# Kernel optimization log

Measured on AMD Instinct MI355X. Metric: run time of the kernel, lower is better.

The kernel has to match this reference:

```python
import jax, jax.numpy as jnp
import numpy as np
import math

HID = 4096
SLOTS = 8
HEADS = 8
BD = 512  # bottleneck_dim
HD = BD // HEADS  # effective head dim = 64
B, S = 4, 4096


def setup_inputs() -> dict:
    key = jax.random.key(0)
    ks = jax.random.split(key, 8)
    std = 1.0 / math.sqrt(HID)
    return {
        "hidden_states": jax.random.normal(ks[0], (B, S, HID), dtype=jnp.float32),
        "attention_mask": jax.random.randint(ks[1], (B, S), 0, 2, dtype=jnp.int32),
        "memory_slots": jax.random.normal(ks[2], (SLOTS, HID), dtype=jnp.float32) * std,
        # torch nn.Linear weights are [out_features, in_features]
        "Wq": jax.random.normal(ks[3], (BD, HID), dtype=jnp.float32) * std,
        "Wk": jax.random.normal(ks[4], (BD, HID), dtype=jnp.float32) * std,
        "Wv": jax.random.normal(ks[5], (BD, HID), dtype=jnp.float32) * std,
        "Wo": jax.random.normal(ks[6], (HID, BD), dtype=jnp.float32) * (1.0 / math.sqrt(BD)),
    }


def reference(hidden_states, attention_mask, memory_slots, Wq, Wk, Wv, Wo):
    # Q from learnable slots (same for every batch element): [slots, BD]
    Q = memory_slots @ Wq.T
    Q = Q.reshape(SLOTS, HEADS, HD)                      # n h d
    # K/V from sequence: [b, s, BD] -> [b, s, h, d]
    K = jnp.einsum('bsi,oi->bso', hidden_states, Wk).reshape(B, S, HEADS, HD)
    V = jnp.einsum('bsi,oi->bso', hidden_states, Wv).reshape(B, S, HEADS, HD)
    # scores: [b, h, n, s]
    scores = jnp.einsum('nhd,bshd->bhns', Q, K) / jnp.sqrt(jnp.array(HD, scores_dtype := jnp.float32))
    mask = attention_mask[:, None, None, :]              # [b,1,1,s]
    scores = jnp.where(mask == 0, jnp.finfo(scores.dtype).min, scores)
    attn = jax.nn.softmax(scores, axis=-1)
    # output: [b, n, h, d] -> [b, n, BD]
    out = jnp.einsum('bhns,bshd->bnhd', attn, V).reshape(B, SLOTS, BD)
    # o_proj back to hidden_size
    return jnp.einsum('bnd,od->bno', out, Wo)            # [b, slots, HID]
```

## Files before the change

### kernel.cpp

```cpp
#include <hip/hip_runtime.h>
#include <math.h>

#define HID   4096
#define SLOTS 8
#define HEADS 8
#define BD    512
#define HD    64
#define BB    4
#define SS    4096
#define R64   64
#define LSTR  72
#define KC    1024
#define NKZ   4
#define NT    16

typedef __attribute__((ext_vector_type(8))) short bf16x8;
typedef __attribute__((ext_vector_type(4))) float f32x4;

__device__ __forceinline__ unsigned short f2bf(float x) {
  unsigned int u = __builtin_bit_cast(unsigned int, x);
  return (unsigned short)((u + 0x7fffu + ((u >> 16) & 1u)) >> 16);
}

__device__ __forceinline__ void gl16(const void* g, void* l) {
  __builtin_amdgcn_global_load_lds(
      (const __attribute__((address_space(1))) unsigned int*)g,
      (__attribute__((address_space(3))) unsigned int*)l, 16, 0, 0);
}

__global__ __launch_bounds__(256) void hsb_kernel(const float* __restrict__ hs,
                                                  unsigned short* __restrict__ hsb) {
  const size_t total = (size_t)BB * SS * HID / 8;
  size_t stride = (size_t)gridDim.x * blockDim.x;
  for (size_t u = (size_t)blockIdx.x * blockDim.x + threadIdx.x; u < total; u += stride) {
    const float* src = hs + u * 8;
    float4 a = *(const float4*)src;
    float4 b = *(const float4*)(src + 4);
    union { unsigned short us[8]; uint4 q; } o;
    o.us[0] = f2bf(a.x); o.us[1] = f2bf(a.y); o.us[2] = f2bf(a.z); o.us[3] = f2bf(a.w);
    o.us[4] = f2bf(b.x); o.us[5] = f2bf(b.y); o.us[6] = f2bf(b.z); o.us[7] = f2bf(b.w);
    *(uint4*)(hsb + u * 8) = o.q;
  }
}

__global__ void q_kernel(const float* __restrict__ ms, const float* __restrict__ Wq,
                         float* __restrict__ Q) {
  int w = (blockIdx.x * blockDim.x + threadIdx.x) >> 6;
  int lane = threadIdx.x & 63;
  if (w >= SLOTS * BD) return;
  int n = w >> 9, o = w & (BD - 1);
  const float* a = ms + n * HID;
  const float* b = Wq + (size_t)o * HID;
  float acc = 0.f;
  for (int i = lane; i < HID; i += 64) acc = fmaf(a[i], b[i], acc);
  #pragma unroll
  for (int off = 32; off; off >>= 1) acc += __shfl_down(acc, off, 64);
  if (lane == 0) Q[w] = acc;
}

__global__ void qw_kernel(const float* __restrict__ Q, const float* __restrict__ Wk,
                          unsigned short* __restrict__ QW) {
  int idx = blockIdx.x * blockDim.x + threadIdx.x;
  int r = idx >> 12, i = idx & (HID - 1);
  int h = r >> 3, n = r & 7;
  const float* q  = Q + n * BD + h * HD;
  const float* wk = Wk + (size_t)(h * HD) * HID + i;
  float acc = 0.f;
  #pragma unroll 8
  for (int d = 0; d < HD; ++d) acc = fmaf(q[d], wk[(size_t)d * HID], acc);
  QW[idx] = f2bf(acc * 0.125f);
}

__global__ __launch_bounds__(256) void scores_mfma(const unsigned short* __restrict__ hsb,
                                                   const unsigned short* __restrict__ QW,
                                                   float* __restrict__ sp) {
  __shared__ __align__(16) unsigned short As[2][4096];
  __shared__ __align__(16) unsigned short Bs[2][4096];
  const int stile = blockIdx.x, b = blockIdx.y, kz = blockIdx.z;
  const int tid = threadIdx.x;
  const int wv = tid >> 6, lane = tid & 63;
  const int quad = lane >> 4, l16 = lane & 15;
  const int trow = tid >> 3;
  const int tslot = (tid & 7) << 4;
  const int scol = tslot ^ ((trow & 7) << 4);
  const char* aSrc0 = (const char*)hsb +
      (((size_t)(b * SS + stile * 64 + trow)) * HID + kz * KC) * 2 + scol;
  const char* aSrc1 = (const char*)hsb +
      (((size_t)(b * SS + stile * 64 + 32 + trow)) * HID + kz * KC) * 2 + scol;
  const char* bSrc0 = (const char*)QW + (((size_t)trow) * HID + kz * KC) * 2 + scol;
  const char* bSrc1 = (const char*)QW + (((size_t)(32 + trow)) * HID + kz * KC) * 2 + scol;

  f32x4 acc[4] = {};
  gl16(aSrc0, &As[0][tid * 8]);
  gl16(aSrc1, &As[0][2048 + tid * 8]);
  gl16(bSrc0, &Bs[0][tid * 8]);
  gl16(bSrc1, &Bs[0][2048 + tid * 8]);
  __syncthreads();

  const int sw = (l16 & 7) << 4;
  for (int c = 0; c < NT; ++c) {
    const int cur = c & 1, nxt = cur ^ 1;
    if (c < NT - 1) {
      const size_t off = (size_t)(c + 1) * 128;
      gl16(aSrc0 + off, &As[nxt][tid * 8]);
      gl16(aSrc1 + off, &As[nxt][2048 + tid * 8]);
      gl16(bSrc0 + off, &Bs[nxt][tid * 8]);
      gl16(bSrc1 + off, &Bs[nxt][2048 + tid * 8]);
    }
    const char* ab = (const char*)&As[cur][0];
    const char* bb = (const char*)&Bs[cur][0];
    #pragma unroll
    for (int ks = 0; ks < 2; ++ks) {
      bf16x8 bfrag = *(const bf16x8*)(bb + (wv * 16 + l16) * 128 + ((ks * 64 + quad * 16) ^ sw));
      #pragma unroll
      for (int mt = 0; mt < 4; ++mt) {
        bf16x8 afrag = *(const bf16x8*)(ab + (mt * 16 + l16) * 128 + ((ks * 64 + quad * 16) ^ sw));
        acc[mt] = __builtin_amdgcn_mfma_f32_16x16x32_bf16(afrag, bfrag, acc[mt], 0, 0, 0);
      }
    }
    __syncthreads();
  }
  const int r = wv * 16 + l16;
  #pragma unroll
  for (int mt = 0; mt < 4; ++mt) {
    int s = stile * 64 + mt * 16 + quad * 4;
    float4 v = make_float4(acc[mt][0], acc[mt][1], acc[mt][2], acc[mt][3]);
    *(float4*)(sp + ((size_t)((kz * BB + b) * R64 + r)) * SS + s) = v;
  }
}

__global__ __launch_bounds__(256) void softmax_kernel(const float* __restrict__ sp,
                                                      const int* __restrict__ mask,
                                                      unsigned short* __restrict__ attn) {
  int br = blockIdx.x;
  int b = br >> 6;
  int tid = threadIdx.x;
  const float* p0 = sp + ((size_t)(0 * BB * R64) + br) * SS;
  const float* p1 = sp + ((size_t)(1 * BB * R64) + br) * SS;
  const float* p2 = sp + ((size_t)(2 * BB * R64) + br) * SS;
  const float* p3 = sp + ((size_t)(3 * BB * R64) + br) * SS;
  const int* mrow = mask + b * SS;
  float vals[16];
  float mx = -INFINITY;
  #pragma unroll
  for (int j = 0; j < 16; ++j) {
    int s = tid + j * 256;
    float v = p0[s] + p1[s] + p2[s] + p3[s];
    if (mrow[s] == 0) v = -INFINITY;
    vals[j] = v;
    mx = fmaxf(mx, v);
  }
  __shared__ float redm[4], reds[4];
  #pragma unroll
  for (int off = 32; off; off >>= 1) mx = fmaxf(mx, __shfl_down(mx, off, 64));
  if ((tid & 63) == 0) redm[tid >> 6] = mx;
  __syncthreads();
  mx = fmaxf(fmaxf(redm[0], redm[1]), fmaxf(redm[2], redm[3]));
  float sum = 0.f;
  #pragma unroll
  for (int j = 0; j < 16; ++j) { vals[j] = expf(vals[j] - mx); sum += vals[j]; }
  #pragma unroll
  for (int off = 32; off; off >>= 1) sum += __shfl_down(sum, off, 64);
  if ((tid & 63) == 0) reds[tid >> 6] = sum;
  __syncthreads();
  sum = reds[0] + reds[1] + reds[2] + reds[3];
  float inv = 1.f / sum;
  #pragma unroll
  for (int j = 0; j < 16; ++j)
    attn[(size_t)br * SS + tid + j * 256] = f2bf(vals[j] * inv);
}

__global__ __launch_bounds__(256) void ctx_mfma(const unsigned short* __restrict__ attn,
                                                const unsigned short* __restrict__ hsb,
                                                float* __restrict__ ctxp) {
  __shared__ __align__(16) unsigned short As[2][4096];
  __shared__ __align__(16) unsigned short Bs[2][64 * LSTR];
  const int itile = blockIdx.x, b = blockIdx.y, kz = blockIdx.z;
  const int tid = threadIdx.x;
  const int wv = tid >> 6, lane = tid & 63;
  const int quad = lane >> 4, l16 = lane & 15;
  const int trow = tid >> 3;
  const int tslot = (tid & 7) << 4;
  const int scol = tslot ^ ((trow & 7) << 4);
  const char* aSrc0 = (const char*)attn +
      (((size_t)(b * R64 + trow)) * SS + kz * KC) * 2 + scol;
  const char* aSrc1 = (const char*)attn +
      (((size_t)(b * R64 + 32 + trow)) * SS + kz * KC) * 2 + scol;
  const int p = tid & 31, g = tid >> 5;
  const unsigned short* hb = hsb + ((size_t)(b * SS + kz * KC + 2 * p)) * HID + itile * 64 + g * 8;

  f32x4 acc[4] = {};
  uint4 h0 = *(const uint4*)(hb);
  uint4 h1 = *(const uint4*)(hb + HID);
  gl16(aSrc0, &As[0][tid * 8]);
  gl16(aSrc1, &As[0][2048 + tid * 8]);
  {
    const unsigned short* u0 = (const unsigned short*)&h0;
    const unsigned short* u1 = (const unsigned short*)&h1;
    unsigned int* bs32 = (unsigned int*)&Bs[0][0];
    #pragma unroll
    for (int j = 0; j < 8; ++j)
      bs32[(g * 8 + j) * (LSTR / 2) + p] = (unsigned int)u0[j] | ((unsigned int)u1[j] << 16);
  }
  h0 = *(const uint4*)(hb + (size_t)64 * HID);
  h1 = *(const uint4*)(hb + (size_t)65 * HID);
  __syncthreads();

  const int sw = (l16 & 7) << 4;
  for (int c = 0; c < NT; ++c) {
    const int cur = c & 1, nxt = cur ^ 1;
    if (c < NT - 1) {
      const size_t off = (size_t)(c + 1) * 128;
      gl16(aSrc0 + off, &As[nxt][tid * 8]);
      gl16(aSrc1 + off, &As[nxt][2048 + tid * 8]);
      const unsigned short* u0 = (const unsigned short*)&h0;
      const unsigned short* u1 = (const unsigned short*)&h1;
      unsigned int* bs32 = (unsigned int*)&Bs[nxt][0];
      #pragma unroll
      for (int j = 0; j < 8; ++j)
        bs32[(g * 8 + j) * (LSTR / 2) + p] = (unsigned int)u0[j] | ((unsigned int)u1[j] << 16);
      if (c < NT - 2) {
        const unsigned short* hn = hb + (size_t)(c + 2) * 64 * HID;
        h0 = *(const uint4*)(hn);
        h1 = *(const uint4*)(hn + HID);
      }
    }
    const char* ab = (const char*)&As[cur][0];
    #pragma unroll
    for (int ks = 0; ks < 2; ++ks) {
      bf16x8 bfrag = *(const bf16x8*)&Bs[cur][(wv * 16 + l16) * LSTR + ks * 32 + quad * 8];
      #pragma unroll
      for (int mt = 0; mt < 4; ++mt) {
        bf16x8 afrag = *(const bf16x8*)(ab + (mt * 16 + l16) * 128 + ((ks * 64 + quad * 16) ^ sw));
        acc[mt] = __builtin_amdgcn_mfma_f32_16x16x32_bf16(afrag, bfrag, acc[mt], 0, 0, 0);
      }
    }
    __syncthreads();
  }
  const int i = itile * 64 + wv * 16 + l16;
  #pragma unroll
  for (int mt = 0; mt < 4; ++mt) {
    int r0 = mt * 16 + quad * 4;
    #pragma unroll
    for (int j = 0; j < 4; ++j)
      ctxp[((size_t)((kz * BB + b) * R64 + r0 + j)) * HID + i] = acc[mt][j];
  }
}

__global__ void ctxsum_kernel(const float* __restrict__ ctxp, float* __restrict__ ctxs) {
  int idx = blockIdx.x * blockDim.x + threadIdx.x;
  const size_t n4 = (size_t)BB * R64 * HID / 4;
  if ((size_t)idx >= n4) return;
  const float4* a = (const float4*)ctxp;
  float4 v0 = a[idx];
  float4 v1 = a[idx + n4];
  float4 v2 = a[idx + 2 * n4];
  float4 v3 = a[idx + 3 * n4];
  float4 r = make_float4(v0.x + v1.x + v2.x + v3.x, v0.y + v1.y + v2.y + v3.y,
                         v0.z + v1.z + v2.z + v3.z, v0.w + v1.w + v2.w + v3.w);
  ((float4*)ctxs)[idx] = r;
}

__global__ void out_kernel(const float* __restrict__ ctx, const float* __restrict__ Wv,
                           float* __restrict__ out) {
  int w = (blockIdx.x * blockDim.x + threadIdx.x) >> 6;
  int lane = threadIdx.x & 63;
  if (w >= BB * BD) return;
  int b = w >> 9, hd = w & 511, h = hd >> 6;
  const float* wvp = Wv + (size_t)hd * HID;
  const float* cb  = ctx + ((size_t)b * R64 + h * 8) * HID;
  float acc[8] = {};
  for (int i = lane; i < HID; i += 64) {
    float wv = wvp[i];
    #pragma unroll
    for (int n = 0; n < 8; ++n) acc[n] = fmaf(cb[(size_t)n * HID + i], wv, acc[n]);
  }
  #pragma unroll
  for (int n = 0; n < 8; ++n) {
    float a = acc[n];
    #pragma unroll
    for (int off = 32; off; off >>= 1) a += __shfl_down(a, off, 64);
    if (lane == 0) out[((size_t)(b * SLOTS + n)) * BD + hd] = a;
  }
}

__global__ void final_kernel(const float* __restrict__ out, const float* __restrict__ Wo,
                             float* __restrict__ y) {
  int w = (blockIdx.x * blockDim.x + threadIdx.x) >> 6;
  int lane = threadIdx.x & 63;
  if (w >= HID) return;
  const float* wo = Wo + (size_t)w * BD;
  float wreg[8];
  #pragma unroll
  for (int j = 0; j < 8; ++j) wreg[j] = wo[lane + j * 64];
  for (int bn = 0; bn < BB * SLOTS; ++bn) {
    const float* orow = out + bn * BD;
    float acc = 0.f;
    #pragma unroll
    for (int j = 0; j < 8; ++j) acc = fmaf(orow[lane + j * 64], wreg[j], acc);
    #pragma unroll
    for (int off = 32; off; off >>= 1) acc += __shfl_down(acc, off, 64);
    if (lane == 0) y[(size_t)bn * HID + w] = acc;
  }
}

extern "C" void kernel_launch(void* const* d_in, const int* in_sizes, int n_in,
                              void* d_out, int out_size, void* d_ws, size_t ws_size,
                              hipStream_t stream) {
  const float* hs   = (const float*)d_in[0];
  const int*   mask = (const int*)d_in[1];
  const float* ms   = (const float*)d_in[2];
  const float* Wq   = (const float*)d_in[3];
  const float* Wk   = (const float*)d_in[4];
  const float* Wv   = (const float*)d_in[5];
  const float* Wo   = (const float*)d_in[6];

  char* ws = (char*)d_ws;
  float*          Q    = (float*)ws;          ws += 4096 * 4;
  unsigned short* QW   = (unsigned short*)ws; ws += R64 * HID * 2;
  unsigned short* hsb  = (unsigned short*)ws; ws += (size_t)BB * SS * HID * 2;
  float*          sp   = (float*)ws;          ws += (size_t)NKZ * BB * R64 * SS * 4;
  unsigned short* attn = (unsigned short*)ws; ws += (size_t)BB * R64 * SS * 2;
  float*          ctxp = (float*)ws;          ws += (size_t)NKZ * BB * R64 * HID * 4;
  float*          ctxs = (float*)ws;          ws += (size_t)BB * R64 * HID * 4;
  float*          out  = (float*)ws;

  hsb_kernel<<<dim3(2048), 256, 0, stream>>>(hs, hsb);
  q_kernel<<<dim3((SLOTS * BD * 64) / 256), 256, 0, stream>>>(ms, Wq, Q);
  qw_kernel<<<dim3((R64 * HID) / 256), 256, 0, stream>>>(Q, Wk, QW);
  scores_mfma<<<dim3(64, 4, 4), 256, 0, stream>>>(hsb, QW, sp);
  softmax_kernel<<<dim3(BB * R64), 256, 0, stream>>>(sp, mask, attn);
  ctx_mfma<<<dim3(64, 4, 4), 256, 0, stream>>>(attn, hsb, ctxp);
  ctxsum_kernel<<<dim3((BB * R64 * HID / 4) / 256), 256, 0, stream>>>(ctxp, ctxs);
  out_kernel<<<dim3((BB * BD * 64) / 256), 256, 0, stream>>>(ctxs, Wv, out);
  final_kernel<<<dim3((HID * 64) / 256), 256, 0, stream>>>(out, Wo, (float*)d_out);
}
```

Baseline: 551.5 us.

## Fuse bf16 conversion into scores GEMM and fold ctx partial sum into out

Removes the standalone fp32-to-bf16 conversion pass. The scores GEMM now loads fp32 hidden states through registers, converts them, writes them into swizzled LDS, and also writes the bf16 copy out for the later ctx GEMM. Removes the ctxsum kernel by having out_kernel add the four split-K partials inline. This saves one full read-write pass over the large activation tensor and two launches. In exchange the A operand no longer uses async global-to-LDS loads, so load latency is exposed through registers, and out_kernel reads four times more ctx data.

```diff
diff --git a/kernel.cpp b/kernel.cpp
--- a/kernel.cpp
+++ b/kernel.cpp
@@ -28,21 +28,6 @@
       (__attribute__((address_space(3))) unsigned int*)l, 16, 0, 0);
 }
 
-__global__ __launch_bounds__(256) void hsb_kernel(const float* __restrict__ hs,
-                                                  unsigned short* __restrict__ hsb) {
-  const size_t total = (size_t)BB * SS * HID / 8;
-  size_t stride = (size_t)gridDim.x * blockDim.x;
-  for (size_t u = (size_t)blockIdx.x * blockDim.x + threadIdx.x; u < total; u += stride) {
-    const float* src = hs + u * 8;
-    float4 a = *(const float4*)src;
-    float4 b = *(const float4*)(src + 4);
-    union { unsigned short us[8]; uint4 q; } o;
-    o.us[0] = f2bf(a.x); o.us[1] = f2bf(a.y); o.us[2] = f2bf(a.z); o.us[3] = f2bf(a.w);
-    o.us[4] = f2bf(b.x); o.us[5] = f2bf(b.y); o.us[6] = f2bf(b.z); o.us[7] = f2bf(b.w);
-    *(uint4*)(hsb + u * 8) = o.q;
-  }
-}
-
 __global__ void q_kernel(const float* __restrict__ ms, const float* __restrict__ Wq,
                          float* __restrict__ Q) {
   int w = (blockIdx.x * blockDim.x + threadIdx.x) >> 6;
@@ -71,8 +56,9 @@
   QW[idx] = f2bf(acc * 0.125f);
 }
 
-__global__ __launch_bounds__(256) void scores_mfma(const unsigned short* __restrict__ hsb,
+__global__ __launch_bounds__(256) void scores_mfma(const float* __restrict__ hs,
                                                    const unsigned short* __restrict__ QW,
+                                                   unsigned short* __restrict__ hsb,
                                                    float* __restrict__ sp) {
   __shared__ __align__(16) unsigned short As[2][4096];
   __shared__ __align__(16) unsigned short Bs[2][4096];
@@ -80,32 +66,66 @@
   const int tid = threadIdx.x;
   const int wv = tid >> 6, lane = tid & 63;
   const int quad = lane >> 4, l16 = lane & 15;
+  const int arow = tid >> 2, acol = (tid & 3) << 4;
+  const float* aSrc = hs + ((size_t)(b * SS + stile * 64 + arow)) * HID + kz * KC + acol;
+  unsigned short* hOut = hsb + ((size_t)(b * SS + stile * 64 + arow)) * HID + kz * KC + acol;
+  const int aswz = (arow & 7) << 4;
+  const int abyte0 = arow * 128 + ((acol * 2) ^ aswz);
+  const int abyte1 = arow * 128 + ((acol * 2 + 16) ^ aswz);
   const int trow = tid >> 3;
   const int tslot = (tid & 7) << 4;
   const int scol = tslot ^ ((trow & 7) << 4);
-  const char* aSrc0 = (const char*)hsb +
-      (((size_t)(b * SS + stile * 64 + trow)) * HID + kz * KC) * 2 + scol;
-  const char* aSrc1 = (const char*)hsb +
-      (((size_t)(b * SS + stile * 64 + 32 + trow)) * HID + kz * KC) * 2 + scol;
   const char* bSrc0 = (const char*)QW + (((size_t)trow) * HID + kz * KC) * 2 + scol;
   const char* bSrc1 = (const char*)QW + (((size_t)(32 + trow)) * HID + kz * KC) * 2 + scol;
 
   f32x4 acc[4] = {};
-  gl16(aSrc0, &As[0][tid * 8]);
-  gl16(aSrc1, &As[0][2048 + tid * 8]);
+  float4 f0 = *(const float4*)(aSrc);
+  float4 f1 = *(const float4*)(aSrc + 4);
+  float4 f2 = *(const float4*)(aSrc + 8);
+  float4 f3 = *(const float4*)(aSrc + 12);
   gl16(bSrc0, &Bs[0][tid * 8]);
   gl16(bSrc1, &Bs[0][2048 + tid * 8]);
+  {
+    union { unsigned short us[16]; uint4 q[2]; } u;
+    float f[16] = {f0.x, f0.y, f0.z, f0.w, f1.x, f1.y, f1.z, f1.w,
+                   f2.x, f2.y, f2.z, f2.w, f3.x, f3.y, f3.z, f3.w};
+    #pragma unroll
+    for (int j = 0; j < 16; ++j) u.us[j] = f2bf(f[j]);
+    *(uint4*)((char*)&As[0][0] + abyte0) = u.q[0];
+    *(uint4*)((char*)&As[0][0] + abyte1) = u.q[1];
+    *(uint4*)(hOut)     = u.q[0];
+    *(uint4*)(hOut + 8) = u.q[1];
+  }
+  f0 = *(const float4*)(aSrc + 64);
+  f1 = *(const float4*)(aSrc + 68);
+  f2 = *(const float4*)(aSrc + 72);
+  f3 = *(const float4*)(aSrc + 76);
   __syncthreads();
 
   const int sw = (l16 & 7) << 4;
   for (int c = 0; c < NT; ++c) {
     const int cur = c & 1, nxt = cur ^ 1;
     if (c < NT - 1) {
-      const size_t off = (size_t)(c + 1) * 128;
-      gl16(aSrc0 + off, &As[nxt][tid * 8]);
-      gl16(aSrc1 + off, &As[nxt][2048 + tid * 8]);
-      gl16(bSrc0 + off, &Bs[nxt][tid * 8]);
-      gl16(bSrc1 + off, &Bs[nxt][2048 + tid * 8]);
+      const size_t boff = (size_t)(c + 1) * 128;
+      gl16(bSrc0 + boff, &Bs[nxt][tid * 8]);
+      gl16(bSrc1 + boff, &Bs[nxt][2048 + tid * 8]);
+      union { unsigned short us[16]; uint4 q[2]; } u;
+      float f[16] = {f0.x, f0.y, f0.z, f0.w, f1.x, f1.y, f1.z, f1.w,
+                     f2.x, f2.y, f2.z, f2.w, f3.x, f3.y, f3.z, f3.w};
+      #pragma unroll
+      for (int j = 0; j < 16; ++j) u.us[j] = f2bf(f[j]);
+      *(uint4*)((char*)&As[nxt][0] + abyte0) = u.q[0];
+      *(uint4*)((char*)&As[nxt][0] + abyte1) = u.q[1];
+      unsigned short* ho = hOut + (size_t)(c + 1) * 64;
+      *(uint4*)(ho)     = u.q[0];
+      *(uint4*)(ho + 8) = u.q[1];
+      if (c < NT - 2) {
+        const float* an = aSrc + (size_t)(c + 2) * 64;
+        f0 = *(const float4*)(an);
+        f1 = *(const float4*)(an + 4);
+        f2 = *(const float4*)(an + 8);
+        f3 = *(const float4*)(an + 12);
+      }
     }
     const char* ab = (const char*)&As[cur][0];
     const char* bb = (const char*)&Bs[cur][0];
@@ -247,33 +267,24 @@
   }
 }
 
-__global__ void ctxsum_kernel(const float* __restrict__ ctxp, float* __restrict__ ctxs) {
-  int idx = blockIdx.x * blockDim.x + threadIdx.x;
-  const size_t n4 = (size_t)BB * R64 * HID / 4;
-  if ((size_t)idx >= n4) return;
-  const float4* a = (const float4*)ctxp;
-  float4 v0 = a[idx];
-  float4 v1 = a[idx + n4];
-  float4 v2 = a[idx + 2 * n4];
-  float4 v3 = a[idx + 3 * n4];
-  float4 r = make_float4(v0.x + v1.x + v2.x + v3.x, v0.y + v1.y + v2.y + v3.y,
-                         v0.z + v1.z + v2.z + v3.z, v0.w + v1.w + v2.w + v3.w);
-  ((float4*)ctxs)[idx] = r;
-}
-
-__global__ void out_kernel(const float* __restrict__ ctx, const float* __restrict__ Wv,
+__global__ void out_kernel(const float* __restrict__ ctxp, const float* __restrict__ Wv,
                            float* __restrict__ out) {
   int w = (blockIdx.x * blockDim.x + threadIdx.x) >> 6;
   int lane = threadIdx.x & 63;
   if (w >= BB * BD) return;
   int b = w >> 9, hd = w & 511, h = hd >> 6;
+  const size_t PSTR = (size_t)BB * R64 * HID;
   const float* wvp = Wv + (size_t)hd * HID;
-  const float* cb  = ctx + ((size_t)b * R64 + h * 8) * HID;
+  const float* cb  = ctxp + ((size_t)b * R64 + h * 8) * HID;
   float acc[8] = {};
   for (int i = lane; i < HID; i += 64) {
     float wv = wvp[i];
     #pragma unroll
-    for (int n = 0; n < 8; ++n) acc[n] = fmaf(cb[(size_t)n * HID + i], wv, acc[n]);
+    for (int n = 0; n < 8; ++n) {
+      size_t o = (size_t)n * HID + i;
+      float v = cb[o] + cb[PSTR + o] + cb[2 * PSTR + o] + cb[3 * PSTR + o];
+      acc[n] = fmaf(v, wv, acc[n]);
+    }
   }
   #pragma unroll
   for (int n = 0; n < 8; ++n) {
@@ -322,16 +333,13 @@
   float*          sp   = (float*)ws;          ws += (size_t)NKZ * BB * R64 * SS * 4;
   unsigned short* attn = (unsigned short*)ws; ws += (size_t)BB * R64 * SS * 2;
   float*          ctxp = (float*)ws;          ws += (size_t)NKZ * BB * R64 * HID * 4;
-  float*          ctxs = (float*)ws;          ws += (size_t)BB * R64 * HID * 4;
   float*          out  = (float*)ws;
 
-  hsb_kernel<<<dim3(2048), 256, 0, stream>>>(hs, hsb);
   q_kernel<<<dim3((SLOTS * BD * 64) / 256), 256, 0, stream>>>(ms, Wq, Q);
   qw_kernel<<<dim3((R64 * HID) / 256), 256, 0, stream>>>(Q, Wk, QW);
-  scores_mfma<<<dim3(64, 4, 4), 256, 0, stream>>>(hsb, QW, sp);
+  scores_mfma<<<dim3(64, 4, 4), 256, 0, stream>>>(hs, QW, hsb, sp);
   softmax_kernel<<<dim3(BB * R64), 256, 0, stream>>>(sp, mask, attn);
   ctx_mfma<<<dim3(64, 4, 4), 256, 0, stream>>>(attn, hsb, ctxp);
-  ctxsum_kernel<<<dim3((BB * R64 * HID / 4) / 256), 256, 0, stream>>>(ctxp, ctxs);
-  out_kernel<<<dim3((BB * BD * 64) / 256), 256, 0, stream>>>(ctxs, Wv, out);
+  out_kernel<<<dim3((BB * BD * 64) / 256), 256, 0, stream>>>(ctxp, Wv, out);
   final_kernel<<<dim3((HID * 64) / 256), 256, 0, stream>>>(out, Wo, (float*)d_out);
 }
```

New measurement: 578.8 us. +5.0%, slower.
